# Optimization experiments

Measured on AMD Instinct MI355X. Metric: run time of the kernel, lower is better.

The kernel has to match this reference:

```python
import jax, jax.numpy as jnp
import numpy as np

B, S, D, F = 4, 2048, 1024, 4096

def setup_inputs() -> dict:
    key = jax.random.key(0)
    ks = jax.random.split(key, 6)
    return {
        "x": jax.random.normal(ks[0], (B, S, D), jnp.float32),
        "Qw": jax.random.normal(ks[1], (D, D), jnp.float32) / 40,
        "Kw": jax.random.normal(ks[2], (D, D), jnp.float32) / 40,
        "Vw": jax.random.normal(ks[3], (D, D), jnp.float32) / 40,
        "w1": jax.random.normal(ks[4], (D, F), jnp.float32) / 40,
        "b1": jnp.zeros((F,), jnp.float32),
        "w2": jax.random.normal(ks[5], (F, D), jnp.float32) / 40,
        "b2": jnp.zeros((D,), jnp.float32),
        "gamma1": jnp.ones((D,), jnp.float32),
        "beta1": jnp.zeros((D,), jnp.float32),
        "gamma2": jnp.ones((D,), jnp.float32),
        "beta2": jnp.zeros((D,), jnp.float32),
    }

def _layernorm(x, gamma, beta):
    num = x - jnp.mean(x, axis=-1, keepdims=True)
    den = jnp.sqrt(jnp.var(x, axis=-1, keepdims=True) + 1e-05)
    return gamma * (num / den) + beta

def _attention(x, Qw, Kw, Vw):
    Q, K, V = x @ Qw, x @ Kw, x @ Vw
    d = x.shape[-1]
    s = x.shape[-2]
    mask = jnp.where(jnp.tril(jnp.ones((s, s))) == 0, -jnp.inf, 0.0)
    scores = Q @ jnp.swapaxes(K, -1, -2) / jnp.sqrt(d) + mask
    return jax.nn.softmax(scores, axis=-1) @ V

def reference(x, Qw, Kw, Vw, w1, b1, w2, b2, gamma1, beta1, gamma2, beta2):
    x = x + _attention(_layernorm(x, gamma1, beta1), Qw, Kw, Vw)
    h = _layernorm(x, gamma2, beta2)
    x = x + (jax.nn.relu(h @ w1 + b1) @ w2 + b2)
    return x
```

## Files before the change

kernel.cpp:

```cpp
#include <hip/hip_runtime.h>
#include <hip/hip_bf16.h>

#define B_ 4
#define S_ 2048
#define D_ 1024
#define F_ 4096

typedef short bf16x8 __attribute__((ext_vector_type(8)));
typedef float f32x4 __attribute__((ext_vector_type(4)));

static __device__ __forceinline__ unsigned short f2bf(float f) {
    union { float f; unsigned int u; } v; v.f = f;
    unsigned int u = v.u + 0x7FFF + ((v.u >> 16) & 1);
    return (unsigned short)(u >> 16);
}
static __device__ __forceinline__ float bf2f(unsigned short u) {
    union { unsigned int u; float f; } v; v.u = ((unsigned int)u) << 16;
    return v.f;
}

typedef const __attribute__((address_space(1))) unsigned int* gp_t;
typedef __attribute__((address_space(3))) unsigned int* lp_t;
static __device__ __forceinline__ void gld16(const unsigned short* g, unsigned short* l) {
    __builtin_amdgcn_global_load_lds((gp_t)g, (lp_t)l, 16, 0, 0);
}

#define WAIT_VM8() __builtin_amdgcn_s_waitcnt(0x0F78)
#define WAIT_VM6() __builtin_amdgcn_s_waitcnt(0x0F76)
#define WAIT_VM0() __builtin_amdgcn_s_waitcnt(0x0F70)

__global__ __launch_bounds__(256) void k_transpose_f32_bf16(
    const float* __restrict__ in, unsigned short* __restrict__ out, int R, int C) {
    __shared__ float t[32][33];
    int c0 = blockIdx.x * 32, r0 = blockIdx.y * 32;
    int x = threadIdx.x, y = threadIdx.y;
#pragma unroll
    for (int i = 0; i < 4; i++)
        t[y + 8 * i][x] = in[(size_t)(r0 + y + 8 * i) * C + c0 + x];
    __syncthreads();
#pragma unroll
    for (int i = 0; i < 4; i++)
        out[(size_t)(c0 + y + 8 * i) * R + r0 + x] = f2bf(t[x][y + 8 * i]);
}

__global__ __launch_bounds__(256) void k_transpose_w3(
    const float* __restrict__ Qw, const float* __restrict__ Kw, const float* __restrict__ Vw,
    unsigned short* __restrict__ out) {
    __shared__ float t[32][33];
    int z = blockIdx.z;
    const float* in = (z == 0) ? Qw : (z == 1) ? Kw : Vw;
    out += (size_t)z * D_ * D_;
    int c0 = blockIdx.x * 32, r0 = blockIdx.y * 32;
    int x = threadIdx.x, y = threadIdx.y;
#pragma unroll
    for (int i = 0; i < 4; i++)
        t[y + 8 * i][x] = in[(size_t)(r0 + y + 8 * i) * D_ + c0 + x];
    __syncthreads();
#pragma unroll
    for (int i = 0; i < 4; i++)
        out[(size_t)(c0 + y + 8 * i) * D_ + r0 + x] = f2bf(t[x][y + 8 * i]);
}

__global__ __launch_bounds__(256) void k_transpose_bf16(
    const unsigned short* __restrict__ in, unsigned short* __restrict__ out,
    int ldin, int ldout, long long szin, long long szout) {
    __shared__ unsigned short t[32][33];
    in += (long long)blockIdx.z * szin;
    out += (long long)blockIdx.z * szout;
    int c0 = blockIdx.x * 32, r0 = blockIdx.y * 32;
    int x = threadIdx.x, y = threadIdx.y;
#pragma unroll
    for (int i = 0; i < 4; i++)
        t[y + 8 * i][x] = in[(size_t)(r0 + y + 8 * i) * ldin + c0 + x];
    __syncthreads();
#pragma unroll
    for (int i = 0; i < 4; i++)
        out[(size_t)(c0 + y + 8 * i) * ldout + r0 + x] = t[x][y + 8 * i];
}

__global__ __launch_bounds__(256) void k_layernorm(
    const float* __restrict__ x, const float* __restrict__ gamma,
    const float* __restrict__ beta, unsigned short* __restrict__ out) {
    int row = blockIdx.x;
    int t = threadIdx.x;
    const float* xr = x + (size_t)row * D_;
    float4 v = ((const float4*)xr)[t];
    float s = v.x + v.y + v.z + v.w;
    float q = v.x * v.x + v.y * v.y + v.z * v.z + v.w * v.w;
#pragma unroll
    for (int off = 32; off; off >>= 1) {
        s += __shfl_down(s, off);
        q += __shfl_down(q, off);
    }
    __shared__ float ls[4], lq[4];
    int wv = t >> 6;
    if ((t & 63) == 0) { ls[wv] = s; lq[wv] = q; }
    __syncthreads();
    if (t == 0) {
        float S = ls[0] + ls[1] + ls[2] + ls[3];
        float Q = lq[0] + lq[1] + lq[2] + lq[3];
        float mean = S * (1.0f / D_);
        float var = Q * (1.0f / D_) - mean * mean;
        ls[0] = mean; lq[0] = rsqrtf(var + 1e-5f);
    }
    __syncthreads();
    float mean = ls[0], rstd = lq[0];
    float4 g = ((const float4*)gamma)[t];
    float4 b = ((const float4*)beta)[t];
    ushort4 o;
    o.x = f2bf(g.x * (v.x - mean) * rstd + b.x);
    o.y = f2bf(g.y * (v.y - mean) * rstd + b.y);
    o.z = f2bf(g.z * (v.z - mean) * rstd + b.z);
    o.w = f2bf(g.w * (v.w - mean) * rstd + b.w);
    ((ushort4*)(out + (size_t)row * D_))[t] = o;
}

__global__ __launch_bounds__(256) void k_softmax(unsigned short* __restrict__ sp) {
    int r = blockIdx.x;
    int i = r & (S_ - 1);
    unsigned short* row = sp + (size_t)r * S_;
    int t = threadIdx.x;
    int valid = i + 1;
    float vals[8];
    float mx = -1e30f;
#pragma unroll
    for (int k = 0; k < 8; k++) {
        int j = t + k * 256;
        vals[k] = (j < valid) ? bf2f(row[j]) : -1e30f;
        mx = fmaxf(mx, vals[k]);
    }
#pragma unroll
    for (int off = 32; off; off >>= 1) mx = fmaxf(mx, __shfl_xor(mx, off));
    __shared__ float red[4];
    if ((t & 63) == 0) red[t >> 6] = mx;
    __syncthreads();
    mx = fmaxf(fmaxf(red[0], red[1]), fmaxf(red[2], red[3]));
    __syncthreads();
    float e[8];
    float sum = 0.f;
#pragma unroll
    for (int k = 0; k < 8; k++) {
        int j = t + k * 256;
        e[k] = (j < valid) ? __expf(vals[k] - mx) : 0.f;
        sum += e[k];
    }
#pragma unroll
    for (int off = 32; off; off >>= 1) sum += __shfl_xor(sum, off);
    if ((t & 63) == 0) red[t >> 6] = sum;
    __syncthreads();
    sum = red[0] + red[1] + red[2] + red[3];
    float inv = 1.0f / sum;
#pragma unroll
    for (int k = 0; k < 8; k++) {
        int j = t + k * 256;
        row[j] = f2bf(e[k] * inv);
    }
}

template <int EPI>
__global__ __launch_bounds__(256) void k_gemm_bt(
    const unsigned short* __restrict__ A, const unsigned short* __restrict__ Bt,
    void* __restrict__ Cv, const float* __restrict__ bias, const float* __restrict__ res,
    int K, int lda, int ldb, int ldc,
    long long sA, long long sB, long long sC, float scale, int klimit, int swz) {
    int bn, bm, z;
    if (swz > 0) {
        int GN = gridDim.x, GM = gridDim.y;
        int L = blockIdx.x + GN * (blockIdx.y + GM * blockIdx.z);
        int rows = gridDim.y * gridDim.z;
        int xcd = L & 7;
        int s = L >> 3;
        int bng = GN / swz;
        int rpg = rows * swz / 8;
        int xg = xcd % swz, yg = xcd / swz;
        int bnl = s % bng;
        int rl = s / bng;
        int row = yg * rpg + rl;
        bn = xg * bng + bnl;
        bm = row % GM;
        z = row / GM;
    } else {
        bn = blockIdx.x; bm = blockIdx.y; z = blockIdx.z;
    }
    if (EPI == 1 && bn > bm) return;
    A += (long long)z * sA;
    Bt += (long long)z * sB;
    long long coff = (long long)z * sC;
    float* Cf = (float*)Cv;
    unsigned short* Cb = (unsigned short*)Cv;

    __shared__ unsigned short As[2][2][128 * 32];
    __shared__ unsigned short Bs[2][2][128 * 32];

    int t = threadIdx.x;
    int l = t & 63, w = t >> 6;
    int wm = (w & 1) * 64, wn = (w >> 1) * 64;
    int lr = l & 15, lq = l >> 4;

    f32x4 acc[4][4];
#pragma unroll
    for (int i = 0; i < 4; i++)
#pragma unroll
        for (int j = 0; j < 4; j++) acc[i][j] = (f32x4){0.f, 0.f, 0.f, 0.f};

    int kend = K;
    if (klimit) { int ke = (bm + 1) * 128; kend = ke < K ? ke : K; }

    int sr = l >> 2;
    int sc = (l & 3) * 8;
    const unsigned short* gA0 = A + (size_t)(bm * 128 + w * 32 + sr) * lda + sc;
    const unsigned short* gA1 = gA0 + (size_t)16 * lda;
    const unsigned short* gB0 = Bt + (size_t)(bn * 128 + w * 32 + sr) * ldb + sc;
    const unsigned short* gB1 = gB0 + (size_t)16 * ldb;

    auto stage = [&](int buf, int k0) {
#pragma unroll
        for (int kc = 0; kc < 2; kc++) {
            int kk = k0 + kc * 32;
            gld16(gA0 + kk, &As[buf][kc][(w * 32) * 32]);
            gld16(gA1 + kk, &As[buf][kc][(w * 32 + 16) * 32]);
            gld16(gB0 + kk, &Bs[buf][kc][(w * 32) * 32]);
            gld16(gB1 + kk, &Bs[buf][kc][(w * 32 + 16) * 32]);
        }
    };

    int NB = kend >> 6;
    stage(0, 0);
    for (int it = 0; it < NB; it++) {
        int cur = it & 1;
        if (it + 1 < NB) {
            stage(1 - cur, (it + 1) * 64);
            WAIT_VM8();
        } else {
            WAIT_VM0();
        }
        __builtin_amdgcn_s_barrier();
#pragma unroll
        for (int kc = 0; kc < 2; kc++) {
            bf16x8 af[4], bf[4];
#pragma unroll
            for (int i = 0; i < 4; i++)
                af[i] = *(const bf16x8*)(&As[cur][kc][(wm + i * 16 + lr) * 32 + lq * 8]);
#pragma unroll
            for (int j = 0; j < 4; j++)
                bf[j] = *(const bf16x8*)(&Bs[cur][kc][(wn + j * 16 + lr) * 32 + lq * 8]);
#pragma unroll
            for (int i = 0; i < 4; i++)
#pragma unroll
                for (int j = 0; j < 4; j++)
                    acc[i][j] = __builtin_amdgcn_mfma_f32_16x16x32_bf16(af[i], bf[j], acc[i][j], 0, 0, 0);
        }
        __builtin_amdgcn_s_barrier();
    }

#pragma unroll
    for (int i = 0; i < 4; i++) {
        int mbase = bm * 128 + wm + i * 16 + lq * 4;
#pragma unroll
        for (int j = 0; j < 4; j++) {
            int n = bn * 128 + wn + j * 16 + lr;
#pragma unroll
            for (int r = 0; r < 4; r++) {
                int m = mbase + r;
                float v = acc[i][j][r];
                long long idx = coff + (long long)m * ldc + n;
                if (EPI == 0) {
                    Cb[idx] = f2bf(v);
                } else if (EPI == 1) {
                    Cb[idx] = f2bf(v * scale);
                } else if (EPI == 2) {
                    Cf[idx] = v + res[idx];
                } else if (EPI == 3) {
                    float u = v + bias[n];
                    Cb[idx] = f2bf(u > 0.f ? u : 0.f);
                } else {
                    Cf[idx] = v + bias[n] + res[idx];
                }
            }
        }
    }
}

template <int EPI>
__global__ __launch_bounds__(512, 2) void k_gemm256(
    const unsigned short* __restrict__ A, const unsigned short* __restrict__ Bt,
    void* __restrict__ Cv, const float* __restrict__ bias, const float* __restrict__ res,
    int K, int lda, int ldb, int ldc,
    long long sA, long long sB, long long sC, float scale, int klimit) {
    int bn = blockIdx.x, bm = blockIdx.y, z = blockIdx.z;
    if (EPI == 1 && bn > bm) return;
    A += (long long)z * sA;
    Bt += (long long)z * sB;
    long long coff = (long long)z * sC;
    float* Cf = (float*)Cv;
    unsigned short* Cb = (unsigned short*)Cv;

    __shared__ unsigned short As[2][2][128 * 64];
    __shared__ unsigned short Bs[2][2][128 * 64];

    int t = threadIdx.x;
    int l = t & 63, w = t >> 6;
    int wmh = w >> 2;
    int wnh = (w >> 1) & 1;
    int bnl = (w & 1) * 64;
    int lr = l & 15, lq = l >> 4;
    int rx = (lr & 7) << 3;
    int c0 = lq * 8;

    f32x4 acc[8][4];
#pragma unroll
    for (int i = 0; i < 8; i++)
#pragma unroll
        for (int j = 0; j < 4; j++) acc[i][j] = (f32x4){0.f, 0.f, 0.f, 0.f};

    int kend = K;
    if (klimit) { int ke = (bm + 1) * 256; kend = ke < K ? ke : K; }
    int NB = kend >> 6;

    int grow = l >> 3;
    int gcol = ((l & 7) * 8) ^ (((l >> 3) & 7) << 3);
    const unsigned short* gA = A + (size_t)(bm * 256 + w * 16 + grow) * lda + gcol;
    const unsigned short* gB = Bt + (size_t)(bn * 256 + w * 16 + grow) * ldb + gcol;

    auto stageA = [&](int buf, int half, int k0) {
        const unsigned short* g = gA + (size_t)(half * 128) * lda + k0;
        unsigned short* s = &As[buf][half][(w * 16) * 64];
        gld16(g, s);
        gld16(g + (size_t)8 * lda, s + 8 * 64);
    };
    auto stageB = [&](int buf, int half, int k0) {
        const unsigned short* g = gB + (size_t)(half * 128) * ldb + k0;
        unsigned short* s = &Bs[buf][half][(w * 16) * 64];
        gld16(g, s);
        gld16(g + (size_t)8 * ldb, s + 8 * 64);
    };

    stageA(0, 0, 0); stageA(0, 1, 0);
    stageB(0, 0, 0); stageB(0, 1, 0);
    int kp = (NB > 1) ? 64 : 0;
    stageB(1, 0, kp); stageB(1, 1, kp); stageA(1, 0, kp);
    WAIT_VM6();
    __builtin_amdgcn_s_barrier();

    bf16x8 aF0[2][4], aF1[2][4], bF[2][4];

    for (int j = 0; j < NB; j++) {
        int b = j & 1;
        int k1 = ((j + 1 < NB) ? (j + 1) : (NB - 1)) << 6;
        int k2 = ((j + 2 < NB) ? (j + 2) : (NB - 1)) << 6;
        const unsigned short* Ah = &As[b][wmh][0];
        const unsigned short* Bh = &Bs[b][wnh][0];

#pragma unroll
        for (int kc = 0; kc < 2; kc++) {
#pragma unroll
            for (int f = 0; f < 4; f++)
                bF[kc][f] = *(const bf16x8*)(Bh + (bnl + f * 16 + lr) * 64 + ((kc * 32 + c0) ^ rx));
#pragma unroll
            for (int f = 0; f < 4; f++)
                aF0[kc][f] = *(const bf16x8*)(Ah + (f * 16 + lr) * 64 + ((kc * 32 + c0) ^ rx));
        }
        stageA(b ^ 1, 1, k1);
        __builtin_amdgcn_s_barrier();
        __builtin_amdgcn_s_setprio(1);
#pragma unroll
        for (int kc = 0; kc < 2; kc++)
#pragma unroll
            for (int i = 0; i < 4; i++)
#pragma unroll
                for (int jn = 0; jn < 2; jn++)
                    acc[i][jn] = __builtin_amdgcn_mfma_f32_16x16x32_bf16(
                        aF0[kc][i], bF[kc][jn], acc[i][jn], 0, 0, 0);
        __builtin_amdgcn_s_setprio(0);
        __builtin_amdgcn_s_barrier();

#pragma unroll
        for (int kc = 0; kc < 2; kc++)
#pragma unroll
            for (int f = 0; f < 4; f++)
                aF1[kc][f] = *(const bf16x8*)(Ah + (64 + f * 16 + lr) * 64 + ((kc * 32 + c0) ^ rx));
        stageB(b, 0, k2);
        __builtin_amdgcn_s_barrier();
        __builtin_amdgcn_s_setprio(1);
#pragma unroll
        for (int kc = 0; kc < 2; kc++)
#pragma unroll
            for (int i = 0; i < 4; i++)
#pragma unroll
                for (int jn = 0; jn < 2; jn++)
                    acc[4 + i][jn] = __builtin_amdgcn_mfma_f32_16x16x32_bf16(
                        aF1[kc][i], bF[kc][jn], acc[4 + i][jn], 0, 0, 0);
        __builtin_amdgcn_s_setprio(0);
        __builtin_amdgcn_s_barrier();

        stageB(b, 1, k2);
        __builtin_amdgcn_s_barrier();
        __builtin_amdgcn_s_setprio(1);
#pragma unroll
        for (int kc = 0; kc < 2; kc++)
#pragma unroll
            for (int i = 0; i < 4; i++)
#pragma unroll
                for (int jn = 0; jn < 2; jn++)
                    acc[4 + i][2 + jn] = __builtin_amdgcn_mfma_f32_16x16x32_bf16(
                        aF1[kc][i], bF[kc][2 + jn], acc[4 + i][2 + jn], 0, 0, 0);
        __builtin_amdgcn_s_setprio(0);
        __builtin_amdgcn_s_barrier();

        stageA(b, 0, k2);
        WAIT_VM6();
        __builtin_amdgcn_s_barrier();
        __builtin_amdgcn_s_setprio(1);
#pragma unroll
        for (int kc = 0; kc < 2; kc++)
#pragma unroll
            for (int i = 0; i < 4; i++)
#pragma unroll
                for (int jn = 0; jn < 2; jn++)
                    acc[i][2 + jn] = __builtin_amdgcn_mfma_f32_16x16x32_bf16(
                        aF0[kc][i], bF[kc][2 + jn], acc[i][2 + jn], 0, 0, 0);
        __builtin_amdgcn_s_setprio(0);
        __builtin_amdgcn_s_barrier();
    }
    WAIT_VM0();

#pragma unroll
    for (int i = 0; i < 8; i++) {
        int mbase = bm * 256 + wmh * 128 + i * 16 + lq * 4;
#pragma unroll
        for (int jn = 0; jn < 4; jn++) {
            int n = bn * 256 + (w & 3) * 64 + jn * 16 + lr;
#pragma unroll
            for (int r = 0; r < 4; r++) {
                int m = mbase + r;
                float v = acc[i][jn][r];
                long long idx = coff + (long long)m * ldc + n;
                if (EPI == 0) {
                    Cb[idx] = f2bf(v);
                } else if (EPI == 1) {
                    Cb[idx] = f2bf(v * scale);
                } else if (EPI == 2) {
                    Cf[idx] = v + res[idx];
                } else if (EPI == 3) {
                    float u = v + bias[n];
                    Cb[idx] = f2bf(u > 0.f ? u : 0.f);
                } else {
                    Cf[idx] = v + bias[n] + res[idx];
                }
            }
        }
    }
}

extern "C" void kernel_launch(void* const* d_in, const int* in_sizes, int n_in,
                              void* d_out, int out_size, void* d_ws, size_t ws_size,
                              hipStream_t stream) {
    const float* x      = (const float*)d_in[0];
    const float* Qw     = (const float*)d_in[1];
    const float* Kw     = (const float*)d_in[2];
    const float* Vw     = (const float*)d_in[3];
    const float* w1     = (const float*)d_in[4];
    const float* b1     = (const float*)d_in[5];
    const float* w2     = (const float*)d_in[6];
    const float* b2     = (const float*)d_in[7];
    const float* gamma1 = (const float*)d_in[8];
    const float* beta1  = (const float*)d_in[9];
    const float* gamma2 = (const float*)d_in[10];
    const float* beta2  = (const float*)d_in[11];
    float* out = (float*)d_out;

    char* ws = (char*)d_ws;
    size_t off = 0;
    auto alloc = [&](size_t bytes) -> void* {
        void* p = ws + off;
        off += (bytes + 255) & ~(size_t)255;
        return p;
    };
    const size_t MN = (size_t)B_ * S_ * D_;
    unsigned short* xn     = (unsigned short*)alloc(MN * 2);
    unsigned short* scoreP = (unsigned short*)alloc((size_t)B_ * S_ * S_ * 2);
    unsigned short* qkv    = (unsigned short*)alloc((size_t)B_ * S_ * 3072 * 2);
    unsigned short* VT     = (unsigned short*)alloc(MN * 2);
    unsigned short* QKVwT  = (unsigned short*)alloc((size_t)3 * D_ * D_ * 2);
    unsigned short* w1T    = (unsigned short*)alloc((size_t)D_ * F_ * 2);
    unsigned short* w2T    = (unsigned short*)alloc((size_t)F_ * D_ * 2);
    unsigned short* mid = qkv;

    dim3 tb(32, 8);
    k_transpose_w3<<<dim3(D_ / 32, D_ / 32, 3), tb, 0, stream>>>(Qw, Kw, Vw, QKVwT);
    k_transpose_f32_bf16<<<dim3(F_ / 32, D_ / 32), tb, 0, stream>>>(w1, w1T, D_, F_);
    k_transpose_f32_bf16<<<dim3(D_ / 32, F_ / 32), tb, 0, stream>>>(w2, w2T, F_, D_);

    k_layernorm<<<B_ * S_, 256, 0, stream>>>(x, gamma1, beta1, xn);

    const int Mtok = B_ * S_;
    k_gemm256<0><<<dim3(3072 / 256, Mtok / 256), 512, 0, stream>>>(
        xn, QKVwT, qkv, nullptr, nullptr, D_, D_, D_, 3072, 0, 0, 0, 1.f, 0);

    k_transpose_bf16<<<dim3(D_ / 32, S_ / 32, B_), tb, 0, stream>>>(
        qkv + 2048, VT, 3072, S_, (long long)S_ * 3072, (long long)D_ * S_);

    k_gemm256<1><<<dim3(S_ / 256, S_ / 256, B_), 512, 0, stream>>>(
        qkv, qkv + 1024, scoreP, nullptr, nullptr, D_, 3072, 3072, S_,
        (long long)S_ * 3072, (long long)S_ * 3072, (long long)S_ * S_, 0.03125f, 0);

    k_softmax<<<B_ * S_, 256, 0, stream>>>(scoreP);

    k_gemm_bt<2><<<dim3(D_ / 128, S_ / 128, B_), 256, 0, stream>>>(
        scoreP, VT, out, nullptr, x, S_, S_, S_, D_,
        (long long)S_ * S_, (long long)D_ * S_, (long long)S_ * D_, 1.f, 1, 2);

    k_layernorm<<<B_ * S_, 256, 0, stream>>>(out, gamma2, beta2, xn);

    k_gemm256<3><<<dim3(F_ / 256, Mtok / 256), 512, 0, stream>>>(
        xn, w1T, mid, b1, nullptr, D_, D_, D_, F_, 0, 0, 0, 1.f, 0);

    k_gemm_bt<4><<<dim3(D_ / 128, Mtok / 128), 256, 0, stream>>>(
        mid, w2T, out, b2, out, F_, F_, F_, D_, 0, 0, 0, 1.f, 0, 2);
}
```

Baseline: 476.9 us.

## Add pipelined 256x128 GEMM kernel for FFN down-projection

```diff
diff --git a/kernel.cpp b/kernel.cpp
--- a/kernel.cpp
+++ b/kernel.cpp
@@ -25,9 +25,11 @@
     __builtin_amdgcn_global_load_lds((gp_t)g, (lp_t)l, 16, 0, 0);
 }
 
-#define WAIT_VM8() __builtin_amdgcn_s_waitcnt(0x0F78)
-#define WAIT_VM6() __builtin_amdgcn_s_waitcnt(0x0F76)
-#define WAIT_VM0() __builtin_amdgcn_s_waitcnt(0x0F70)
+#define WAIT_VM8()   __builtin_amdgcn_s_waitcnt(0x0F78)
+#define WAIT_VM6()   __builtin_amdgcn_s_waitcnt(0x0F76)
+#define WAIT_VM4()   __builtin_amdgcn_s_waitcnt(0x0F74)
+#define WAIT_VM0()   __builtin_amdgcn_s_waitcnt(0x0F70)
+#define WAIT_LGKM0() __builtin_amdgcn_s_waitcnt(0xC07F)
 
 __global__ __launch_bounds__(256) void k_transpose_f32_bf16(
     const float* __restrict__ in, unsigned short* __restrict__ out, int R, int C) {
@@ -452,6 +454,169 @@
     }
 }
 
+template <int EPI>
+__global__ __launch_bounds__(512, 2) void k_gemm_b128(
+    const unsigned short* __restrict__ A, const unsigned short* __restrict__ Bt,
+    void* __restrict__ Cv, const float* __restrict__ bias, const float* __restrict__ res,
+    int K, int lda, int ldb, int ldc,
+    long long sA, long long sB, long long sC, float scale, int klimit) {
+    int bn = blockIdx.x, bm = blockIdx.y, z = blockIdx.z;
+    A += (long long)z * sA;
+    Bt += (long long)z * sB;
+    long long coff = (long long)z * sC;
+    float* Cf = (float*)Cv;
+    unsigned short* Cb = (unsigned short*)Cv;
+
+    __shared__ unsigned short As[2][2][128 * 64];
+    __shared__ unsigned short Bs[2][128 * 64];
+
+    int t = threadIdx.x;
+    int l = t & 63, w = t >> 6;
+    int wq = w >> 1;
+    int wnn = w & 1;
+    int ah = wq >> 1;
+    int mb = (wq & 1) * 64;
+    int bnl = wnn * 64;
+    int lr = l & 15, lq = l >> 4;
+    int rx = (lr & 7) << 3;
+    int c0 = lq * 8;
+
+    f32x4 acc[4][4];
+#pragma unroll
+    for (int i = 0; i < 4; i++)
+#pragma unroll
+        for (int j = 0; j < 4; j++) acc[i][j] = (f32x4){0.f, 0.f, 0.f, 0.f};
+
+    int kend = K;
+    if (klimit) { int ke = (bm + 1) * 256; kend = ke < K ? ke : K; }
+    int NB = kend >> 6;
+
+    int grow = l >> 3;
+    int gcol = ((l & 7) * 8) ^ (((l >> 3) & 7) << 3);
+    const unsigned short* gA = A + (size_t)(bm * 256 + w * 16 + grow) * lda + gcol;
+    const unsigned short* gB = Bt + (size_t)(bn * 128 + w * 16 + grow) * ldb + gcol;
+
+    auto stageA = [&](int buf, int half, int k0) {
+        const unsigned short* g = gA + (size_t)(half * 128) * lda + k0;
+        unsigned short* s = &As[buf][half][(w * 16) * 64];
+        gld16(g, s);
+        gld16(g + (size_t)8 * lda, s + 8 * 64);
+    };
+    auto stageB = [&](int buf, int k0) {
+        const unsigned short* g = gB + k0;
+        unsigned short* s = &Bs[buf][(w * 16) * 64];
+        gld16(g, s);
+        gld16(g + (size_t)8 * ldb, s + 8 * 64);
+    };
+
+    stageA(0, 0, 0); stageA(0, 1, 0); stageB(0, 0);
+    if (NB > 1) {
+        stageB(1, 64); stageA(1, 0, 64);
+        WAIT_VM4();
+    } else {
+        WAIT_VM0();
+    }
+    __builtin_amdgcn_s_barrier();
+
+    bf16x8 aF0[2][2], aF1[2][2], bF[2][4];
+
+    for (int j = 0; j < NB; j++) {
+        int b = j & 1;
+        const unsigned short* Ah = &As[b][ah][0];
+        const unsigned short* Bh = &Bs[b][0];
+
+#pragma unroll
+        for (int kc = 0; kc < 2; kc++) {
+#pragma unroll
+            for (int f = 0; f < 4; f++)
+                bF[kc][f] = *(const bf16x8*)(Bh + (bnl + f * 16 + lr) * 64 + ((kc * 32 + c0) ^ rx));
+#pragma unroll
+            for (int f = 0; f < 2; f++)
+                aF0[kc][f] = *(const bf16x8*)(Ah + (mb + f * 16 + lr) * 64 + ((kc * 32 + c0) ^ rx));
+        }
+        if (j + 1 < NB) stageA(b ^ 1, 1, (j + 1) << 6);
+        WAIT_LGKM0();
+        __builtin_amdgcn_s_barrier();
+        __builtin_amdgcn_s_setprio(1);
+#pragma unroll
+        for (int kc = 0; kc < 2; kc++)
+#pragma unroll
+            for (int i = 0; i < 2; i++)
+#pragma unroll
+                for (int jn = 0; jn < 2; jn++)
+                    acc[i][jn] = __builtin_amdgcn_mfma_f32_16x16x32_bf16(
+                        aF0[kc][i], bF[kc][jn], acc[i][jn], 0, 0, 0);
+        __builtin_amdgcn_s_setprio(0);
+        __builtin_amdgcn_s_barrier();
+
+#pragma unroll
+        for (int kc = 0; kc < 2; kc++)
+#pragma unroll
+            for (int f = 0; f < 2; f++)
+                aF1[kc][f] = *(const bf16x8*)(Ah + (mb + 32 + f * 16 + lr) * 64 + ((kc * 32 + c0) ^ rx));
+        if (j + 2 < NB) stageB(b, (j + 2) << 6);
+        __builtin_amdgcn_s_barrier();
+        __builtin_amdgcn_s_setprio(1);
+#pragma unroll
+        for (int kc = 0; kc < 2; kc++)
+#pragma unroll
+            for (int i = 0; i < 2; i++)
+#pragma unroll
+                for (int jn = 0; jn < 4; jn++)
+                    acc[2 + i][jn] = __builtin_amdgcn_mfma_f32_16x16x32_bf16(
+                        aF1[kc][i], bF[kc][jn], acc[2 + i][jn], 0, 0, 0);
+        __builtin_amdgcn_s_setprio(0);
+        __builtin_amdgcn_s_barrier();
+
+        if (j + 2 < NB) {
+            stageA(b, 0, (j + 2) << 6);
+            WAIT_VM4();
+        } else {
+            WAIT_VM0();
+        }
+        __builtin_amdgcn_s_barrier();
+        __builtin_amdgcn_s_setprio(1);
+#pragma unroll
+        for (int kc = 0; kc < 2; kc++)
+#pragma unroll
+            for (int i = 0; i < 2; i++)
+#pragma unroll
+                for (int jn = 0; jn < 2; jn++)
+                    acc[i][2 + jn] = __builtin_amdgcn_mfma_f32_16x16x32_bf16(
+                        aF0[kc][i], bF[kc][2 + jn], acc[i][2 + jn], 0, 0, 0);
+        __builtin_amdgcn_s_setprio(0);
+        __builtin_amdgcn_s_barrier();
+    }
+    WAIT_VM0();
+
+#pragma unroll
+    for (int i = 0; i < 4; i++) {
+        int mbase = bm * 256 + ah * 128 + mb + i * 16 + lq * 4;
+#pragma unroll
+        for (int jn = 0; jn < 4; jn++) {
+            int n = bn * 128 + bnl + jn * 16 + lr;
+#pragma unroll
+            for (int r = 0; r < 4; r++) {
+                int m = mbase + r;
+                float v = acc[i][jn][r];
+                long long idx = coff + (long long)m * ldc + n;
+                if (EPI == 0) {
+                    Cb[idx] = f2bf(v);
+                } else if (EPI == 1) {
+                    Cb[idx] = f2bf(v * scale);
+                } else if (EPI == 2) {
+                    Cf[idx] = v + res[idx];
+                } else if (EPI == 3) {
+                    float u = v + bias[n];
+                    Cb[idx] = f2bf(u > 0.f ? u : 0.f);
+                } else {
+                    Cf[idx] = v + bias[n] + res[idx];
+                }
+            }
+        }
+    }
+}
+
 extern "C" void kernel_launch(void* const* d_in, const int* in_sizes, int n_in,
                               void* d_out, int out_size, void* d_ws, size_t ws_size,
                               hipStream_t stream) {
@@ -515,6 +680,6 @@
     k_gemm256<3><<<dim3(F_ / 256, Mtok / 256), 512, 0, stream>>>(
         xn, w1T, mid, b1, nullptr, D_, D_, D_, F_, 0, 0, 0, 1.f, 0);
 
-    k_gemm_bt<4><<<dim3(D_ / 128, Mtok / 128), 256, 0, stream>>>(
-        mid, w2T, out, b2, out, F_, F_, F_, D_, 0, 0, 0, 1.f, 0, 2);
-}
+    k_gemm_b128<4><<<dim3(D_ / 128, Mtok / 256), 512, 0, stream>>>(
+        mid, w2T, out, b2, out, F_, F_, F_, D_, 0, 0, 0, 1.f, 0);
+}
```

After: 493.9 us. 1.04x slower.
